# Performance work log

Measured on AMD Instinct MI355X. Metric: run time of the kernel, lower is better.

The kernel has to match this reference:

```python
import jax, jax.numpy as jnp
import numpy as np

N, E, D, H, L = 40000, 640000, 128, 4, 2
C = D // H  # head dim
NEG_SLOPE = 0.2


def setup_inputs() -> dict:
    key = jax.random.key(0)
    ks = jax.random.split(key, 9)
    s = 1.0 / np.sqrt(D)
    x = jax.random.normal(ks[0], (N, D), dtype=jnp.float32)
    edge_index = jax.random.randint(ks[1], (2, E), 0, N, dtype=jnp.int64)
    # Per-layer stacked GATv2Conv parameters (PyG parameterization):
    Wl = jax.random.normal(ks[2], (L, D, D), dtype=jnp.float32) * s   # lin_l weight
    bl = jnp.zeros((L, D), dtype=jnp.float32)                          # lin_l bias
    Wr = jax.random.normal(ks[3], (L, D, D), dtype=jnp.float32) * s   # lin_r weight
    br = jnp.zeros((L, D), dtype=jnp.float32)                          # lin_r bias
    att = jax.random.normal(ks[4], (L, H, C), dtype=jnp.float32) * (1.0 / np.sqrt(C))
    Wres = jax.random.normal(ks[5], (L, D, D), dtype=jnp.float32) * s  # residual proj
    bias = jnp.zeros((L, D), dtype=jnp.float32)                        # final bias
    return {"x": x, "edge_index": edge_index, "Wl": Wl, "bl": bl,
            "Wr": Wr, "br": br, "att": att, "Wres": Wres, "bias": bias}


def _gatv2_layer(x, src, dst, Wl, bl, Wr, br, att, Wres, b):
    # x: [N, D]; src/dst: [E] (edge j -> i, dst is aggregation target)
    xl = (x @ Wl + bl).reshape(N, H, C)
    xr = (x @ Wr + br).reshape(N, H, C)
    # per-edge GATv2 score: a^T LeakyReLU(xl_j + xr_i)
    e = jax.nn.leaky_relu(xl[src] + xr[dst], NEG_SLOPE)        # [E, H, C]
    alpha = jnp.einsum('ehc,hc->eh', e, att)                    # [E, H]
    # segment softmax over edges grouped by target node
    amax = jax.ops.segment_max(alpha, dst, num_segments=N)      # [N, H]
    amax = jnp.where(jnp.isfinite(amax), amax, 0.0)
    ex = jnp.exp(alpha - amax[dst])
    denom = jax.ops.segment_sum(ex, dst, num_segments=N) + 1e-16
    a = ex / denom[dst]                                         # [E, H]
    # scatter-add weighted source messages
    out = jax.ops.segment_sum(xl[src] * a[:, :, None], dst, num_segments=N)
    out = out.reshape(N, H * C) + x @ Wres + b                  # concat heads + residual + bias
    return jax.nn.elu(out)


def reference(x, edge_index, Wl, bl, Wr, br, att, Wres, bias):
    src, dst = edge_index[0], edge_index[1]
    for l in range(L):
        x = _gatv2_layer(x, src, dst, Wl[l], bl[l], Wr[l], br[l], att[l], Wres[l], bias[l])
    return x
```

## Files before the change

### kernel.cpp

```cpp
#include <hip/hip_runtime.h>
#include <cstdint>

#define NN 40000
#define EE 640000
#define DD 128
#define HH 4
#define CC 32
#define LL 2
#define NEG_SLOPE 0.2f
#define NBLK 157

typedef __attribute__((ext_vector_type(8))) short bf16x8;
typedef __attribute__((ext_vector_type(4))) float f32x4;
typedef __attribute__((ext_vector_type(2))) float f32x2;

__device__ __forceinline__ unsigned short f2bf(float f) {
    unsigned u = __float_as_uint(f);
    unsigned r = (u + 0x7FFFu + ((u >> 16) & 1)) >> 16;
    return (unsigned short)r;
}
__device__ __forceinline__ float bf2f(unsigned short u) {
    return __uint_as_float(((unsigned)u) << 16);
}

__device__ __forceinline__ void gload16(const void* g, void* l) {
    __builtin_amdgcn_global_load_lds(
        (const __attribute__((address_space(1))) unsigned*)g,
        (__attribute__((address_space(3))) unsigned*)l, 16, 0, 0);
}

template<int CTRL>
__device__ __forceinline__ float dpp_badd(float v) {
    const int j = __builtin_amdgcn_mov_dpp(__float_as_int(v), CTRL, 0xF, 0xF, true);
    return v + __int_as_float(j);
}

__global__ __launch_bounds__(256) void prep_kernel(
    const float* __restrict__ x,
    const float* __restrict__ Wl, const float* __restrict__ Wr,
    const float* __restrict__ Wres,
    unsigned short* __restrict__ xb, unsigned short* __restrict__ Wb,
    int* __restrict__ deg)
{
    const int i = blockIdx.x * 256 + threadIdx.x;
    if (i < NN * DD / 4) {
        const float4 v = ((const float4*)x)[i];
        ushort4 o;
        o.x = f2bf(v.x); o.y = f2bf(v.y); o.z = f2bf(v.z); o.w = f2bf(v.w);
        ((ushort4*)xb)[i] = o;
    }
    if (i < LL * 6 * 8192) {
        const int l = i / 49152;
        const int rem0 = i - l * 49152;
        const int nb = rem0 >> 13;
        const int rem = rem0 & 8191;
        const int q = rem >> 9;
        const int n = (rem >> 3) & 63;
        const int j = rem & 7;
        const int k = q * 8 + j;
        const int colg = (nb & 1) * 64 + n;
        const float* W = (nb < 2) ? Wl : (nb < 4) ? Wr : Wres;
        Wb[i] = f2bf(W[(size_t)l * DD * DD + k * DD + colg]);
    }
    if (i < NN) deg[i] = 0;
}

__global__ __launch_bounds__(256) void gemm_mfma_kernel(
    const unsigned short* __restrict__ xb, const unsigned short* __restrict__ Wb,
    const float* __restrict__ bl, const float* __restrict__ br,
    const float* __restrict__ bias,
    unsigned short* __restrict__ xlb, unsigned short* __restrict__ xrb,
    unsigned short* __restrict__ resb)
{
    __shared__ __align__(16) unsigned short lds[16384];
    const int lane = threadIdx.x & 63;
    const int wv = threadIdx.x >> 6;
    const int row0 = blockIdx.x << 6;

#pragma unroll
    for (int j = 0; j < 4; ++j) {
        const int q = j * 4 + wv;
        gload16(xb + (size_t)(row0 + lane) * DD + q * 8, &lds[q * 512]);
    }

    const int wm = wv >> 1, wn = wv & 1;
    const int h = lane >> 4, r = lane & 15;

    for (int t = 0; t < 6; ++t) {
        __syncthreads();
#pragma unroll
        for (int j = 0; j < 4; ++j) {
            const int q = j * 4 + wv;
            gload16(Wb + (size_t)t * 8192 + q * 512 + lane * 8, &lds[8192 + q * 512]);
        }
        __syncthreads();

        f32x4 acc[2][2] = {{{0.f,0.f,0.f,0.f},{0.f,0.f,0.f,0.f}},
                           {{0.f,0.f,0.f,0.f},{0.f,0.f,0.f,0.f}}};
#pragma unroll
        for (int s = 0; s < 4; ++s) {
            const int base = (s * 4 + h) * 64;
            const bf16x8 a0 = *(const bf16x8*)&lds[(base + wm * 32 + r) * 8];
            const bf16x8 a1 = *(const bf16x8*)&lds[(base + wm * 32 + 16 + r) * 8];
            const bf16x8 b0 = *(const bf16x8*)&lds[8192 + (base + wn * 32 + r) * 8];
            const bf16x8 b1 = *(const bf16x8*)&lds[8192 + (base + wn * 32 + 16 + r) * 8];
            acc[0][0] = __builtin_amdgcn_mfma_f32_16x16x32_bf16(a0, b0, acc[0][0], 0, 0, 0);
            acc[0][1] = __builtin_amdgcn_mfma_f32_16x16x32_bf16(a0, b1, acc[0][1], 0, 0, 0);
            acc[1][0] = __builtin_amdgcn_mfma_f32_16x16x32_bf16(a1, b0, acc[1][0], 0, 0, 0);
            acc[1][1] = __builtin_amdgcn_mfma_f32_16x16x32_bf16(a1, b1, acc[1][1], 0, 0, 0);
        }

        unsigned short* const outp = (t < 2) ? xlb : (t < 4) ? xrb : resb;
        const float* const bp = (t < 2) ? bl : (t < 4) ? br : bias;
        const int c0 = (t & 1) * 64 + wn * 32;
#pragma unroll
        for (int ni = 0; ni < 2; ++ni) {
            const int col = c0 + ni * 16 + r;
            const float bv = bp[col];
#pragma unroll
            for (int mi = 0; mi < 2; ++mi) {
                const int rw = row0 + wm * 32 + mi * 16 + h * 4;
#pragma unroll
                for (int v = 0; v < 4; ++v)
                    outp[(size_t)(rw + v) * DD + col] = f2bf(acc[mi][ni][v] + bv);
            }
        }
    }
}


__global__ __launch_bounds__(256) void hist_kernel(
    const int* __restrict__ dst, int* __restrict__ deg)
{
    const int e = blockIdx.x * 256 + threadIdx.x;
    if (e < EE) atomicAdd(&deg[dst[e]], 1);
}

__global__ __launch_bounds__(256) void scan1_kernel(
    const int* __restrict__ deg, int* __restrict__ rowptr, int* __restrict__ blksum)
{
    __shared__ int s[256];
    const int i = blockIdx.x * 256 + threadIdx.x;
    const int v = (i < NN) ? deg[i] : 0;
    s[threadIdx.x] = v;
    __syncthreads();
    for (int off = 1; off < 256; off <<= 1) {
        const int t = (threadIdx.x >= off) ? s[threadIdx.x - off] : 0;
        __syncthreads();
        s[threadIdx.x] += t;
        __syncthreads();
    }
    if (i < NN) rowptr[i] = s[threadIdx.x] - v;
    if (threadIdx.x == 255) blksum[blockIdx.x] = s[255];
}

__global__ __launch_bounds__(256) void scan23_kernel(
    int* __restrict__ rowptr, const int* __restrict__ blksum, int* __restrict__ cursor)
{
    __shared__ int s[256];
    const int v = (threadIdx.x < NBLK) ? blksum[threadIdx.x] : 0;
    s[threadIdx.x] = v;
    __syncthreads();
    for (int off = 1; off < 256; off <<= 1) {
        const int t = (threadIdx.x >= off) ? s[threadIdx.x - off] : 0;
        __syncthreads();
        s[threadIdx.x] += t;
        __syncthreads();
    }
    const int boff = s[blockIdx.x] - blksum[blockIdx.x];
    const int i = blockIdx.x * 256 + threadIdx.x;
    if (i < NN) {
        const int val = rowptr[i] + boff;
        rowptr[i] = val;
        cursor[i] = val;
    }
    if (i == 0) rowptr[NN] = EE;
}

__global__ __launch_bounds__(256) void fill_kernel(
    const int* __restrict__ src, const int* __restrict__ dst,
    int* __restrict__ cursor, int* __restrict__ colb)
{
    const int e = blockIdx.x * 256 + threadIdx.x;
    if (e < EE) {
        const int p = atomicAdd(&cursor[dst[e]], 1);
        colb[p] = src[e] << 8;
    }
}

__global__ __launch_bounds__(256) void gather_kernel(
    const unsigned short* __restrict__ xlb, const unsigned short* __restrict__ xrb,
    const unsigned short* __restrict__ resb,
    const int* __restrict__ rowptr, const int* __restrict__ colb,
    const float* __restrict__ att,
    float* __restrict__ outf, unsigned short* __restrict__ outb)
{
    const int node = (blockIdx.x * 256 + threadIdx.x) >> 6;
    const int lane = threadIdx.x & 63;
    if (node >= NN) return;
    const int halfid = lane >> 5;
    const int hl = lane & 31;

    const uint2 xu = *(const uint2*)(xrb + (size_t)node * DD + hl * 4);
    const f32x2 xr01 = {__uint_as_float(xu.x << 16), __uint_as_float(xu.x & 0xFFFF0000u)};
    const f32x2 xr23 = {__uint_as_float(xu.y << 16), __uint_as_float(xu.y & 0xFFFF0000u)};
    const float4 attv = ((const float4*)att)[hl];
    const f32x2 at6_01 = {0.6f * attv.x, 0.6f * attv.y};
    const f32x2 at6_23 = {0.6f * attv.z, 0.6f * attv.w};
    const f32x2 at4_01 = {0.4f * attv.x, 0.4f * attv.y};
    const f32x2 at4_23 = {0.4f * attv.z, 0.4f * attv.w};
    const char* const xbase = (const char*)xlb;

    float d = 0.f;
    f32x2 acc01 = {0.f, 0.f}, acc23 = {0.f, 0.f};
    const int beg = rowptr[node], end = rowptr[node + 1];

    int p = beg;

#define CHUNK_BODY(GUARDED)                                                    \
    {                                                                          \
        f32x2 xv01[4], xv23[4]; float al[4]; int vl[4];                        \
        _Pragma("unroll")                                                      \
        for (int i = 0; i < 4; ++i) {                                          \
            const int q = p + 2 * i + halfid;                                  \
            vl[i] = GUARDED ? (q < end) : 1;                                   \
            const int off = colb[vl[i] ? q : beg];                             \
            const uint2 u = *(const uint2*)(xbase + off + hl * 8);             \
            xv01[i] = (f32x2){__uint_as_float(u.x << 16),                      \
                              __uint_as_float(u.x & 0xFFFF0000u)};             \
            xv23[i] = (f32x2){__uint_as_float(u.y << 16),                      \
                              __uint_as_float(u.y & 0xFFFF0000u)};             \
        }                                                                      \
        _Pragma("unroll")                                                      \
        for (int i = 0; i < 4; ++i) {                                          \
            const f32x2 z01 = xv01[i] + xr01;                                  \
            const f32x2 z23 = xv23[i] + xr23;                                  \
            const f32x2 za01 = __builtin_elementwise_abs(z01);                 \
            const f32x2 za23 = __builtin_elementwise_abs(z23);                 \
            f32x2 s2 = z01 * at6_01;                                           \
            s2 += za01 * at4_01;                                               \
            s2 += z23 * at6_23;                                                \
            s2 += za23 * at4_23;                                               \
            al[i] = s2.x + s2.y;                                               \
        }                                                                      \
        _Pragma("unroll")                                                      \
        for (int i = 0; i < 4; ++i) {                                          \
            al[i] = dpp_badd<0xB1>(al[i]);      \
            al[i] = dpp_badd<0x4E>(al[i]);      \
            al[i] = dpp_badd<0x141>(al[i]);     \
        }                                                                      \
        _Pragma("unroll")                                                      \
        for (int i = 0; i < 4; ++i) {                                          \
            float w = __expf(al[i]);                                           \
            if (GUARDED) w = vl[i] ? w : 0.f;                                  \
            const f32x2 w2 = {w, w};                                           \
            d += w;                                                            \
            acc01 += w2 * xv01[i];                                             \
            acc23 += w2 * xv23[i];                                             \
        }                                                                      \
    }

    for (; p + 8 <= end; p += 8) CHUNK_BODY(0)
    if (p < end) CHUNK_BODY(1)
#undef CHUNK_BODY

    d += __shfl_xor(d, 32);
    acc01.x += __shfl_xor(acc01.x, 32); acc01.y += __shfl_xor(acc01.y, 32);
    acc23.x += __shfl_xor(acc23.x, 32); acc23.y += __shfl_xor(acc23.y, 32);

    if (halfid == 0) {
        const float inv = 1.f / (d + 1e-16f);
        const ushort4 ru = ((const ushort4*)(resb + (size_t)node * DD))[hl];
        float o0 = acc01.x * inv + bf2f(ru.x);
        float o1 = acc01.y * inv + bf2f(ru.y);
        float o2 = acc23.x * inv + bf2f(ru.z);
        float o3 = acc23.y * inv + bf2f(ru.w);
        o0 = (o0 > 0.f) ? o0 : expm1f(o0);
        o1 = (o1 > 0.f) ? o1 : expm1f(o1);
        o2 = (o2 > 0.f) ? o2 : expm1f(o2);
        o3 = (o3 > 0.f) ? o3 : expm1f(o3);
        if (outf) {
            float4 ov; ov.x = o0; ov.y = o1; ov.z = o2; ov.w = o3;
            ((float4*)(outf + (size_t)node * DD))[hl] = ov;
        }
        if (outb) {
            ushort4 ob;
            ob.x = f2bf(o0); ob.y = f2bf(o1); ob.z = f2bf(o2); ob.w = f2bf(o3);
            ((ushort4*)(outb + (size_t)node * DD))[hl] = ob;
        }
    }
}

extern "C" void kernel_launch(void* const* d_in, const int* in_sizes, int n_in,
                              void* d_out, int out_size, void* d_ws, size_t ws_size,
                              hipStream_t stream)
{
    const float* x0   = (const float*)d_in[0];
    const int*   ei   = (const int*)  d_in[1];
    const float* Wl   = (const float*)d_in[2];
    const float* bl   = (const float*)d_in[3];
    const float* Wr   = (const float*)d_in[4];
    const float* br   = (const float*)d_in[5];
    const float* att  = (const float*)d_in[6];
    const float* Wres = (const float*)d_in[7];
    const float* bias = (const float*)d_in[8];
    const int* src = ei;
    const int* dst = ei + EE;

    float* p = (float*)d_ws;
    unsigned short* xlb  = (unsigned short*)p; p += (size_t)NN * DD / 2;
    unsigned short* xrb  = (unsigned short*)p; p += (size_t)NN * DD / 2;
    unsigned short* resb = (unsigned short*)p; p += (size_t)NN * DD / 2;
    unsigned short* xb0  = (unsigned short*)p; p += (size_t)NN * DD / 2;
    unsigned short* xb1  = (unsigned short*)p; p += (size_t)NN * DD / 2;
    unsigned short* Wb   = (unsigned short*)p; p += LL * 6 * 8192 / 2;
    int* rowptr = (int*)p; p += NN + 1;
    int* deg    = (int*)p; p += NN;
    int* cursor = (int*)p; p += NN;
    int* blksum = (int*)p; p += NBLK;
    int* colb   = (int*)p; p += EE;

    prep_kernel<<<(NN * DD / 4 + 255) / 256, 256, 0, stream>>>(
        x0, Wl, Wr, Wres, xb0, Wb, deg);
    hist_kernel<<<(EE + 255) / 256, 256, 0, stream>>>(dst, deg);
    scan1_kernel<<<NBLK, 256, 0, stream>>>(deg, rowptr, blksum);
    scan23_kernel<<<NBLK, 256, 0, stream>>>(rowptr, blksum, cursor);
    fill_kernel<<<(EE + 255) / 256, 256, 0, stream>>>(src, dst, cursor, colb);

    for (int l = 0; l < LL; ++l) {
        const unsigned short* xin = (l == 0) ? xb0 : xb1;
        gemm_mfma_kernel<<<625, 256, 0, stream>>>(
            xin, Wb + (size_t)l * 6 * 8192, bl + l * DD, br + l * DD, bias + l * DD,
            xlb, xrb, resb);
        gather_kernel<<<(NN * 64 + 255) / 256, 256, 0, stream>>>(
            xlb, xrb, resb, rowptr, colb, att + (size_t)l * HH * CC,
            (l == LL - 1) ? (float*)d_out : nullptr,
            (l == 0) ? xb1 : nullptr);
    }
}
```

Measured before the change: 170.4 us.

## Double-buffer GEMM weight tiles and software-prefetch gathered rows in aggregation

The GEMM kernel now stages two weight tiles at a time into a double-buffered LDS region (80 KB), loading the next pair while the current pair feeds the MFMAs. This removes one barrier per tile and hides global-load latency. The edge aggregation kernel adds register prefetch of the next 8-edge chunk of gathered xl rows before computing the current chunk, to overlap gather latency with the math. The larger LDS footprint and extra live registers may lower occupancy in both kernels.

New measurement: 175.1 us. 2.8% more time.

```diff
diff --git a/kernel.cpp b/kernel.cpp
--- a/kernel.cpp
+++ b/kernel.cpp
@@ -72,7 +72,7 @@
     unsigned short* __restrict__ xlb, unsigned short* __restrict__ xrb,
     unsigned short* __restrict__ resb)
 {
-    __shared__ __align__(16) unsigned short lds[16384];
+    __shared__ __align__(16) unsigned short lds[40960];
     const int lane = threadIdx.x & 63;
     const int wv = threadIdx.x >> 6;
     const int row0 = blockIdx.x << 6;
@@ -82,47 +82,65 @@
         const int q = j * 4 + wv;
         gload16(xb + (size_t)(row0 + lane) * DD + q * 8, &lds[q * 512]);
     }
+#pragma unroll
+    for (int j = 0; j < 4; ++j) {
+        const int q = j * 4 + wv;
+#pragma unroll
+        for (int tt = 0; tt < 2; ++tt)
+            gload16(Wb + (size_t)tt * 8192 + q * 512 + lane * 8,
+                    &lds[8192 + tt * 8192 + q * 512]);
+    }
 
     const int wm = wv >> 1, wn = wv & 1;
     const int h = lane >> 4, r = lane & 15;
 
-    for (int t = 0; t < 6; ++t) {
+    for (int it = 0; it < 3; ++it) {
         __syncthreads();
-#pragma unroll
-        for (int j = 0; j < 4; ++j) {
-            const int q = j * 4 + wv;
-            gload16(Wb + (size_t)t * 8192 + q * 512 + lane * 8, &lds[8192 + q * 512]);
-        }
-        __syncthreads();
-
-        f32x4 acc[2][2] = {{{0.f,0.f,0.f,0.f},{0.f,0.f,0.f,0.f}},
-                           {{0.f,0.f,0.f,0.f},{0.f,0.f,0.f,0.f}}};
-#pragma unroll
-        for (int s = 0; s < 4; ++s) {
-            const int base = (s * 4 + h) * 64;
-            const bf16x8 a0 = *(const bf16x8*)&lds[(base + wm * 32 + r) * 8];
-            const bf16x8 a1 = *(const bf16x8*)&lds[(base + wm * 32 + 16 + r) * 8];
-            const bf16x8 b0 = *(const bf16x8*)&lds[8192 + (base + wn * 32 + r) * 8];
-            const bf16x8 b1 = *(const bf16x8*)&lds[8192 + (base + wn * 32 + 16 + r) * 8];
-            acc[0][0] = __builtin_amdgcn_mfma_f32_16x16x32_bf16(a0, b0, acc[0][0], 0, 0, 0);
-            acc[0][1] = __builtin_amdgcn_mfma_f32_16x16x32_bf16(a0, b1, acc[0][1], 0, 0, 0);
-            acc[1][0] = __builtin_amdgcn_mfma_f32_16x16x32_bf16(a1, b0, acc[1][0], 0, 0, 0);
-            acc[1][1] = __builtin_amdgcn_mfma_f32_16x16x32_bf16(a1, b1, acc[1][1], 0, 0, 0);
-        }
-
-        unsigned short* const outp = (t < 2) ? xlb : (t < 4) ? xrb : resb;
-        const float* const bp = (t < 2) ? bl : (t < 4) ? br : bias;
-        const int c0 = (t & 1) * 64 + wn * 32;
-#pragma unroll
-        for (int ni = 0; ni < 2; ++ni) {
-            const int col = c0 + ni * 16 + r;
-            const float bv = bp[col];
-#pragma unroll
-            for (int mi = 0; mi < 2; ++mi) {
-                const int rw = row0 + wm * 32 + mi * 16 + h * 4;
-#pragma unroll
-                for (int v = 0; v < 4; ++v)
-                    outp[(size_t)(rw + v) * DD + col] = f2bf(acc[mi][ni][v] + bv);
+        if (it < 2) {
+            const int P = it + 1;
+            const int bufN = 8192 + (P & 1) * 16384;
+#pragma unroll
+            for (int j = 0; j < 4; ++j) {
+                const int q = j * 4 + wv;
+#pragma unroll
+                for (int tt = 0; tt < 2; ++tt)
+                    gload16(Wb + (size_t)(2 * P + tt) * 8192 + q * 512 + lane * 8,
+                            &lds[bufN + tt * 8192 + q * 512]);
+            }
+        }
+        const int bufC = 8192 + (it & 1) * 16384;
+#pragma unroll
+        for (int tt = 0; tt < 2; ++tt) {
+            const int t = it * 2 + tt;
+            f32x4 acc[2][2] = {{{0.f,0.f,0.f,0.f},{0.f,0.f,0.f,0.f}},
+                               {{0.f,0.f,0.f,0.f},{0.f,0.f,0.f,0.f}}};
+#pragma unroll
+            for (int s = 0; s < 4; ++s) {
+                const int base = (s * 4 + h) * 64;
+                const bf16x8 a0 = *(const bf16x8*)&lds[(base + wm * 32 + r) * 8];
+                const bf16x8 a1 = *(const bf16x8*)&lds[(base + wm * 32 + 16 + r) * 8];
+                const bf16x8 b0 = *(const bf16x8*)&lds[bufC + tt * 8192 + (base + wn * 32 + r) * 8];
+                const bf16x8 b1 = *(const bf16x8*)&lds[bufC + tt * 8192 + (base + wn * 32 + 16 + r) * 8];
+                acc[0][0] = __builtin_amdgcn_mfma_f32_16x16x32_bf16(a0, b0, acc[0][0], 0, 0, 0);
+                acc[0][1] = __builtin_amdgcn_mfma_f32_16x16x32_bf16(a0, b1, acc[0][1], 0, 0, 0);
+                acc[1][0] = __builtin_amdgcn_mfma_f32_16x16x32_bf16(a1, b0, acc[1][0], 0, 0, 0);
+                acc[1][1] = __builtin_amdgcn_mfma_f32_16x16x32_bf16(a1, b1, acc[1][1], 0, 0, 0);
+            }
+
+            unsigned short* const outp = (t < 2) ? xlb : (t < 4) ? xrb : resb;
+            const float* const bp = (t < 2) ? bl : (t < 4) ? br : bias;
+            const int c0 = (t & 1) * 64 + wn * 32;
+#pragma unroll
+            for (int ni = 0; ni < 2; ++ni) {
+                const int col = c0 + ni * 16 + r;
+                const float bv = bp[col];
+#pragma unroll
+                for (int mi = 0; mi < 2; ++mi) {
+                    const int rw = row0 + wm * 32 + mi * 16 + h * 4;
+#pragma unroll
+                    for (int v = 0; v < 4; ++v)
+                        outp[(size_t)(rw + v) * DD + col] = f2bf(acc[mi][ni][v] + bv);
+                }
             }
         }
     }
@@ -214,55 +232,106 @@
     float d = 0.f;
     f32x2 acc01 = {0.f, 0.f}, acc23 = {0.f, 0.f};
     const int beg = rowptr[node], end = rowptr[node + 1];
+    const int nfull = (end - beg) >> 3;
 
     int p = beg;
-
-#define CHUNK_BODY(GUARDED)                                                    \
-    {                                                                          \
-        f32x2 xv01[4], xv23[4]; float al[4]; int vl[4];                        \
-        _Pragma("unroll")                                                      \
-        for (int i = 0; i < 4; ++i) {                                          \
-            const int q = p + 2 * i + halfid;                                  \
-            vl[i] = GUARDED ? (q < end) : 1;                                   \
-            const int off = colb[vl[i] ? q : beg];                             \
-            const uint2 u = *(const uint2*)(xbase + off + hl * 8);             \
-            xv01[i] = (f32x2){__uint_as_float(u.x << 16),                      \
-                              __uint_as_float(u.x & 0xFFFF0000u)};             \
-            xv23[i] = (f32x2){__uint_as_float(u.y << 16),                      \
-                              __uint_as_float(u.y & 0xFFFF0000u)};             \
-        }                                                                      \
-        _Pragma("unroll")                                                      \
-        for (int i = 0; i < 4; ++i) {                                          \
-            const f32x2 z01 = xv01[i] + xr01;                                  \
-            const f32x2 z23 = xv23[i] + xr23;                                  \
-            const f32x2 za01 = __builtin_elementwise_abs(z01);                 \
-            const f32x2 za23 = __builtin_elementwise_abs(z23);                 \
-            f32x2 s2 = z01 * at6_01;                                           \
-            s2 += za01 * at4_01;                                               \
-            s2 += z23 * at6_23;                                                \
-            s2 += za23 * at4_23;                                               \
-            al[i] = s2.x + s2.y;                                               \
-        }                                                                      \
-        _Pragma("unroll")                                                      \
-        for (int i = 0; i < 4; ++i) {                                          \
-            al[i] = dpp_badd<0xB1>(al[i]);      \
-            al[i] = dpp_badd<0x4E>(al[i]);      \
-            al[i] = dpp_badd<0x141>(al[i]);     \
-        }                                                                      \
-        _Pragma("unroll")                                                      \
-        for (int i = 0; i < 4; ++i) {                                          \
-            float w = __expf(al[i]);                                           \
-            if (GUARDED) w = vl[i] ? w : 0.f;                                  \
-            const f32x2 w2 = {w, w};                                           \
-            d += w;                                                            \
-            acc01 += w2 * xv01[i];                                             \
-            acc23 += w2 * xv23[i];                                             \
-        }                                                                      \
-    }
-
-    for (; p + 8 <= end; p += 8) CHUNK_BODY(0)
-    if (p < end) CHUNK_BODY(1)
-#undef CHUNK_BODY
+    uint2 cu[4];
+    if (nfull > 0) {
+#pragma unroll
+        for (int i = 0; i < 4; ++i) {
+            const int off = colb[p + 2 * i + halfid];
+            cu[i] = *(const uint2*)(xbase + off + hl * 8);
+        }
+    }
+    for (int c = 0; c < nfull; ++c) {
+        uint2 nu[4] = {};
+        if (c + 1 < nfull) {
+            const int pn = p + 8;
+#pragma unroll
+            for (int i = 0; i < 4; ++i) {
+                const int off = colb[pn + 2 * i + halfid];
+                nu[i] = *(const uint2*)(xbase + off + hl * 8);
+            }
+        }
+        f32x2 xv01[4], xv23[4]; float al[4];
+#pragma unroll
+        for (int i = 0; i < 4; ++i) {
+            xv01[i] = (f32x2){__uint_as_float(cu[i].x << 16),
+                              __uint_as_float(cu[i].x & 0xFFFF0000u)};
+            xv23[i] = (f32x2){__uint_as_float(cu[i].y << 16),
+                              __uint_as_float(cu[i].y & 0xFFFF0000u)};
+        }
+#pragma unroll
+        for (int i = 0; i < 4; ++i) {
+            const f32x2 z01 = xv01[i] + xr01;
+            const f32x2 z23 = xv23[i] + xr23;
+            const f32x2 za01 = __builtin_elementwise_abs(z01);
+            const f32x2 za23 = __builtin_elementwise_abs(z23);
+            f32x2 s2 = z01 * at6_01;
+            s2 += za01 * at4_01;
+            s2 += z23 * at6_23;
+            s2 += za23 * at4_23;
+            al[i] = s2.x + s2.y;
+        }
+#pragma unroll
+        for (int i = 0; i < 4; ++i) {
+            al[i] = dpp_badd<0xB1>(al[i]);
+            al[i] = dpp_badd<0x4E>(al[i]);
+            al[i] = dpp_badd<0x141>(al[i]);
+        }
+#pragma unroll
+        for (int i = 0; i < 4; ++i) {
+            const float w = __expf(al[i]);
+            const f32x2 w2 = {w, w};
+            d += w;
+            acc01 += w2 * xv01[i];
+            acc23 += w2 * xv23[i];
+        }
+#pragma unroll
+        for (int i = 0; i < 4; ++i) cu[i] = nu[i];
+        p += 8;
+    }
+    if (p < end) {
+        f32x2 xv01[4], xv23[4]; float al[4]; int vl[4];
+#pragma unroll
+        for (int i = 0; i < 4; ++i) {
+            const int q = p + 2 * i + halfid;
+            vl[i] = (q < end);
+            const int off = colb[vl[i] ? q : beg];
+            const uint2 u = *(const uint2*)(xbase + off + hl * 8);
+            xv01[i] = (f32x2){__uint_as_float(u.x << 16),
+                              __uint_as_float(u.x & 0xFFFF0000u)};
+            xv23[i] = (f32x2){__uint_as_float(u.y << 16),
+                              __uint_as_float(u.y & 0xFFFF0000u)};
+        }
+#pragma unroll
+        for (int i = 0; i < 4; ++i) {
+            const f32x2 z01 = xv01[i] + xr01;
+            const f32x2 z23 = xv23[i] + xr23;
+            const f32x2 za01 = __builtin_elementwise_abs(z01);
+            const f32x2 za23 = __builtin_elementwise_abs(z23);
+            f32x2 s2 = z01 * at6_01;
+            s2 += za01 * at4_01;
+            s2 += z23 * at6_23;
+            s2 += za23 * at4_23;
+            al[i] = s2.x + s2.y;
+        }
+#pragma unroll
+        for (int i = 0; i < 4; ++i) {
+            al[i] = dpp_badd<0xB1>(al[i]);
+            al[i] = dpp_badd<0x4E>(al[i]);
+            al[i] = dpp_badd<0x141>(al[i]);
+        }
+#pragma unroll
+        for (int i = 0; i < 4; ++i) {
+            float w = __expf(al[i]);
+            w = vl[i] ? w : 0.f;
+            const f32x2 w2 = {w, w};
+            d += w;
+            acc01 += w2 * xv01[i];
+            acc23 += w2 * xv23[i];
+        }
+    }
 
     d += __shfl_xor(d, 32);
     acc01.x += __shfl_xor(acc01.x, 32); acc01.y += __shfl_xor(acc01.y, 32);
```
